# Optimization experiments

Measured on AMD Instinct MI355X. Metric: run time of the kernel, lower is better.

The kernel has to match this reference:

```python
import jax
import jax.numpy as jnp
import numpy as np
from jax import lax


def setup_inputs() -> dict:
    key = jax.random.key(0)
    k0, k1 = jax.random.split(key)
    B, C, H, W = 8, 256, 96, 96
    FM0 = jax.random.normal(k0, (B, C, H, W), dtype=jnp.float32)
    FM1 = jax.random.normal(k1, (B, C, H, W), dtype=jnp.float32)
    return {"FM0": FM0, "FM1": FM1, "d_max": 4, "stride": 1}


def pointwise_correlation(FM0, FM1, d_max, stride):
    """out[b,h,w,i,j] = sum_c FM0[b,c,h,w] * FM1[b,c,h+(i-d)*s, w+(j-d)*s],
    with zero padding outside FM1's spatial extent."""
    B, C, H, W = FM0.shape
    D = 2 * d_max + 1
    p = d_max * stride
    FM1p = jnp.pad(FM1, ((0, 0), (0, 0), (p, p), (p, p)))
    offs = jnp.arange(D, dtype=jnp.int32) * stride  # start offsets into padded map
    ys, xs = jnp.meshgrid(offs, offs, indexing="ij")
    offsets = jnp.stack([ys.ravel(), xs.ravel()], axis=-1)  # (D*D, 2)

    def step(carry, off):
        sl = lax.dynamic_slice(FM1p, (0, 0, off[0], off[1]), (B, C, H, W))
        corr = jnp.einsum("bchw,bchw->bhw", FM0, sl)
        return carry, corr

    _, out = lax.scan(step, None, offsets)  # (D*D, B, H, W)
    out = out.reshape(D, D, B, H, W).transpose(2, 3, 4, 0, 1)  # (B, H, W, D, D)
    return out


def reference(FM0, FM1, d_max, stride):
    return pointwise_correlation(FM0, FM1, d_max, stride)
```

## Files before the change

kernel.cpp:

```cpp
#include <hip/hip_runtime.h>

#define HH 96
#define WW 96
#define CC 256
#define PLANE (HH * WW)
#define PITCH 40
#define AROWS 144
#define BROWS 704
#define NGRP 1696
#define NOUT 81

typedef __attribute__((ext_vector_type(4))) float f32x4;
typedef __attribute__((ext_vector_type(2))) unsigned int u32x2;
typedef __attribute__((ext_vector_type(8))) __bf16 bf16x8;

static __device__ __forceinline__ unsigned int pkbf(float x, float y) {
  unsigned int ux = __builtin_bit_cast(unsigned int, x) + 0x8000u;
  unsigned int uy = __builtin_bit_cast(unsigned int, y) + 0x8000u;
  return __builtin_amdgcn_perm(uy, ux, 0x07060302u);
}

__global__ __launch_bounds__(384, 2) void corr_kernel(
    const float* __restrict__ fm0, const float* __restrict__ fm1,
    float* __restrict__ out) {
  __shared__ __align__(16) unsigned short lds[(AROWS + BROWS) * PITCH];

  const int tid = threadIdx.x;
  const int bid = blockIdx.x;
  const int b = bid & 7;
  const int q = bid >> 3;
  const int s = q & 1;
  const int h0 = 3 * (q >> 1);

  const int lane = tid & 63;
  const int wv = tid >> 6;
  const int mm = lane & 15;
  const int kg = lane >> 4;

  const size_t boff = (size_t)b * CC * PLANE;

  if (wv >= 3) {
    const int pt = tid - 192;
    const float* gptr[9];
    int gdst[9];
    bool gact[9], gok[9];
    #pragma unroll
    for (int j = 0; j < 9; ++j) {
      const int g = pt + 192 * j;
      gact[j] = (g < NGRP);
      if (g < 288) {
        const int a = g / 96, r = g % 96;
        const int wq = r >> 3, cq = r & 7;
        const int wst = 48 * s + 4 * wq;
        gok[j] = gact[j];
        gdst[j] = (a * 48 + 4 * wq) * PITCH + 4 * cq;
        gptr[j] = fm0 + boff + (size_t)(4 * cq) * PLANE + (h0 + a) * WW + wst;
      } else {
        const int gb = g - 288;
        const int i = gb >> 7, r = gb & 127;
        const int wq = r >> 3, cq = r & 7;
        const int hb = h0 - 4 + i;
        const int wst = 48 * s - 8 + 4 * wq;
        const bool ok = (hb >= 0) && (hb < HH) && (wst >= 0) && (wst < WW);
        gok[j] = ok && gact[j];
        gdst[j] = (AROWS + i * 64 + 4 * wq) * PITCH + 4 * cq;
        gptr[j] = fm1 + boff + (size_t)(4 * cq) * PLANE +
                  (size_t)(ok ? hb : 0) * WW + (ok ? wst : 0);
      }
    }
    f32x4 pre[9][4];
    #pragma unroll
    for (int j = 0; j < 9; ++j)
      #pragma unroll
      for (int cc = 0; cc < 4; ++cc) pre[j][cc] = f32x4{0.f, 0.f, 0.f, 0.f};
    #pragma unroll
    for (int j = 0; j < 9; ++j)
      if (gok[j]) {
        #pragma unroll
        for (int cc = 0; cc < 4; ++cc)
          pre[j][cc] = *(const f32x4*)(gptr[j] + (size_t)cc * PLANE);
      }

    #pragma unroll 1
    for (int ks = 0; ks < 8; ++ks) {
      __syncthreads();
      #pragma unroll
      for (int j = 0; j < 9; ++j)
        if (gact[j]) {
          #pragma unroll
          for (int dw = 0; dw < 4; ++dw) {
            u32x2 v;
            v.x = pkbf(pre[j][0][dw], pre[j][1][dw]);
            v.y = pkbf(pre[j][2][dw], pre[j][3][dw]);
            *(u32x2*)&lds[gdst[j] + dw * PITCH] = v;
          }
        }
      if (ks < 7) {
        const size_t koff = (size_t)((ks + 1) * 32) * PLANE;
        #pragma unroll
        for (int j = 0; j < 9; ++j)
          if (gok[j]) {
            #pragma unroll
            for (int cc = 0; cc < 4; ++cc)
              pre[j][cc] = *(const f32x4*)(gptr[j] + koff + (size_t)cc * PLANE);
          }
      }
      __syncthreads();
    }
  } else {
    f32x4 acc[9][3][2];
    #pragma unroll
    for (int i = 0; i < 9; ++i)
      #pragma unroll
      for (int mt = 0; mt < 3; ++mt) {
        acc[i][mt][0] = f32x4{0.f, 0.f, 0.f, 0.f};
        acc[i][mt][1] = f32x4{0.f, 0.f, 0.f, 0.f};
      }
    const int abase = (wv * 48 + mm) * PITCH + kg * 8;
    const int bbase = (AROWS + mm) * PITCH + kg * 8;

    #pragma unroll 1
    for (int ks = 0; ks < 8; ++ks) {
      __syncthreads();
      __syncthreads();
      bf16x8 af[3];
      #pragma unroll
      for (int mt = 0; mt < 3; ++mt)
        af[mt] = *(const bf16x8*)&lds[abase + 16 * mt * PITCH];
      #pragma unroll
      for (int i = 0; i < 9; ++i) {
        const int bb = bbase + (wv + i) * 64 * PITCH;
        bf16x8 b0 = *(const bf16x8*)&lds[bb];
        #pragma unroll
        for (int mt = 0; mt < 3; ++mt) {
          bf16x8 b1 = *(const bf16x8*)&lds[bb + 16 * (mt + 1) * PITCH];
          acc[i][mt][0] = __builtin_amdgcn_mfma_f32_16x16x32_bf16(af[mt], b0, acc[i][mt][0], 0, 0, 0);
          acc[i][mt][1] = __builtin_amdgcn_mfma_f32_16x16x32_bf16(af[mt], b1, acc[i][mt][1], 0, 0, 0);
          b0 = b1;
        }
      }
    }

    float* outb = out + ((size_t)b * PLANE + (size_t)(h0 + wv) * WW) * NOUT;
    #pragma unroll
    for (int u = 0; u < 2; ++u)
      #pragma unroll
      for (int rg = 0; rg < 4; ++rg) {
        const int j = 16 * u + mm - 4 * kg - rg - 4;
        if ((unsigned)j < 9u) {
          #pragma unroll
          for (int i = 0; i < 9; ++i)
            #pragma unroll
            for (int mt = 0; mt < 3; ++mt) {
              const int w = 48 * s + 16 * mt + 4 * kg + rg;
              outb[(size_t)w * NOUT + i * 9 + j] = acc[i][mt][u][rg];
            }
        }
      }
  }
}

extern "C" void kernel_launch(void* const* d_in, const int* in_sizes, int n_in,
                              void* d_out, int out_size, void* d_ws, size_t ws_size,
                              hipStream_t stream) {
  const float* fm0 = (const float*)d_in[0];
  const float* fm1 = (const float*)d_in[1];
  float* out = (float*)d_out;
  corr_kernel<<<dim3(512), dim3(384), 0, stream>>>(fm0, fm1, out);
}
```

Measured before the change: 214.4 us.

## Double-buffer LDS so producer waves fill next K-slice while MFMA waves compute

Switches the warp-specialized kernel from a single LDS buffer with two barriers per K-step to two LDS buffers with one barrier per step. The producer waves pack and store slice ks+1 while the consumer waves run MFMAs on slice ks, and the global prefetch moves two slices ahead. The goal is to remove the serialization between the LDS fill phase and the compute phase. The cost is twice the LDS footprint (about 135 KB per block), which may reduce occupancy from two blocks per CU to one.

```diff
diff --git a/kernel.cpp b/kernel.cpp
--- a/kernel.cpp
+++ b/kernel.cpp
@@ -7,7 +7,7 @@
 #define PITCH 40
 #define AROWS 144
 #define BROWS 704
-#define NGRP 1696
+#define LDSN ((AROWS + BROWS) * PITCH)
 #define NOUT 81
 
 typedef __attribute__((ext_vector_type(4))) float f32x4;
@@ -20,10 +20,12 @@
   return __builtin_amdgcn_perm(uy, ux, 0x07060302u);
 }
 
+#define BAR_LGKM() asm volatile("s_waitcnt lgkmcnt(0)\n\ts_barrier" ::: "memory")
+
 __global__ __launch_bounds__(384, 2) void corr_kernel(
     const float* __restrict__ fm0, const float* __restrict__ fm1,
     float* __restrict__ out) {
-  __shared__ __align__(16) unsigned short lds[(AROWS + BROWS) * PITCH];
+  __shared__ __align__(16) unsigned short lds[2 * LDSN];
 
   const int tid = threadIdx.x;
   const int bid = blockIdx.x;
@@ -47,7 +49,7 @@
     #pragma unroll
     for (int j = 0; j < 9; ++j) {
       const int g = pt + 192 * j;
-      gact[j] = (g < NGRP);
+      gact[j] = (g < 1696);
       if (g < 288) {
         const int a = g / 96, r = g % 96;
         const int wq = r >> 3, cq = r & 7;
@@ -68,11 +70,13 @@
                   (size_t)(ok ? hb : 0) * WW + (ok ? wst : 0);
       }
     }
+
     f32x4 pre[9][4];
     #pragma unroll
     for (int j = 0; j < 9; ++j)
       #pragma unroll
       for (int cc = 0; cc < 4; ++cc) pre[j][cc] = f32x4{0.f, 0.f, 0.f, 0.f};
+
     #pragma unroll
     for (int j = 0; j < 9; ++j)
       if (gok[j]) {
@@ -80,23 +84,45 @@
         for (int cc = 0; cc < 4; ++cc)
           pre[j][cc] = *(const f32x4*)(gptr[j] + (size_t)cc * PLANE);
       }
+    #pragma unroll
+    for (int j = 0; j < 9; ++j)
+      if (gact[j]) {
+        #pragma unroll
+        for (int dw = 0; dw < 4; ++dw) {
+          u32x2 v;
+          v.x = pkbf(pre[j][0][dw], pre[j][1][dw]);
+          v.y = pkbf(pre[j][2][dw], pre[j][3][dw]);
+          *(u32x2*)&lds[gdst[j] + dw * PITCH] = v;
+        }
+      }
+    #pragma unroll
+    for (int j = 0; j < 9; ++j)
+      if (gok[j]) {
+        #pragma unroll
+        for (int cc = 0; cc < 4; ++cc)
+          pre[j][cc] = *(const f32x4*)(gptr[j] + (size_t)(32) * PLANE +
+                                       (size_t)cc * PLANE);
+      }
+    BAR_LGKM();
 
     #pragma unroll 1
     for (int ks = 0; ks < 8; ++ks) {
-      __syncthreads();
-      #pragma unroll
-      for (int j = 0; j < 9; ++j)
-        if (gact[j]) {
-          #pragma unroll
-          for (int dw = 0; dw < 4; ++dw) {
-            u32x2 v;
-            v.x = pkbf(pre[j][0][dw], pre[j][1][dw]);
-            v.y = pkbf(pre[j][2][dw], pre[j][3][dw]);
-            *(u32x2*)&lds[gdst[j] + dw * PITCH] = v;
+      if (ks < 7) {
+        const int bo = ((ks + 1) & 1) * LDSN;
+        #pragma unroll
+        for (int j = 0; j < 9; ++j)
+          if (gact[j]) {
+            #pragma unroll
+            for (int dw = 0; dw < 4; ++dw) {
+              u32x2 v;
+              v.x = pkbf(pre[j][0][dw], pre[j][1][dw]);
+              v.y = pkbf(pre[j][2][dw], pre[j][3][dw]);
+              *(u32x2*)&lds[bo + gdst[j] + dw * PITCH] = v;
+            }
           }
-        }
-      if (ks < 7) {
-        const size_t koff = (size_t)((ks + 1) * 32) * PLANE;
+      }
+      if (ks < 6) {
+        const size_t koff = (size_t)((ks + 2) * 32) * PLANE;
         #pragma unroll
         for (int j = 0; j < 9; ++j)
           if (gok[j]) {
@@ -105,7 +131,7 @@
               pre[j][cc] = *(const f32x4*)(gptr[j] + koff + (size_t)cc * PLANE);
           }
       }
-      __syncthreads();
+      BAR_LGKM();
     }
   } else {
     f32x4 acc[9][3][2];
@@ -119,17 +145,18 @@
     const int abase = (wv * 48 + mm) * PITCH + kg * 8;
     const int bbase = (AROWS + mm) * PITCH + kg * 8;
 
+    asm volatile("s_barrier" ::: "memory");
+
     #pragma unroll 1
     for (int ks = 0; ks < 8; ++ks) {
-      __syncthreads();
-      __syncthreads();
+      const int bo = (ks & 1) * LDSN;
       bf16x8 af[3];
       #pragma unroll
       for (int mt = 0; mt < 3; ++mt)
-        af[mt] = *(const bf16x8*)&lds[abase + 16 * mt * PITCH];
+        af[mt] = *(const bf16x8*)&lds[bo + abase + 16 * mt * PITCH];
       #pragma unroll
       for (int i = 0; i < 9; ++i) {
-        const int bb = bbase + (wv + i) * 64 * PITCH;
+        const int bb = bo + bbase + (wv + i) * 64 * PITCH;
         bf16x8 b0 = *(const bf16x8*)&lds[bb];
         #pragma unroll
         for (int mt = 0; mt < 3; ++mt) {
@@ -139,6 +166,7 @@
           b0 = b1;
         }
       }
+      BAR_LGKM();
     }
 
     float* outb = out + ((size_t)b * PLANE + (size_t)(h0 + wv) * WW) * NOUT;
```

Result: slower. 233.8 us (+9.0%).
